# Performance work log

Measured on AMD Instinct MI355X. Metric: run time of the kernel, lower is better.

Reference implementation:

```python
import jax, jax.numpy as jnp
import numpy as np

T = 0.1  # temperature
NEG_M = 1.0


def _normalize(v):
    return v / jnp.linalg.norm(v, axis=1, keepdims=True)


def setup_inputs() -> dict:
    key = jax.random.key(0)
    k1, k2 = jax.random.split(key)
    f1 = _normalize(jax.random.normal(k1, (4096, 128), dtype=jnp.float32))
    f2 = _normalize(jax.random.normal(k2, (4096, 128), dtype=jnp.float32))
    return {"f1": f1, "f2": f2, "dd": 1}


def reference(f1, f2, dd):
    # x: [N, D] with N = 2*B; dd is unused (matches original forward)
    x = jnp.concatenate([f1, f2], axis=0)
    N = x.shape[0]
    half = N // 2
    # positive pairs: (i, i+half) and (i+half, i)
    reordered = jnp.concatenate([x[half:], x[:half]], axis=0)
    # original uses .data (detached) on the second operand
    pos = jnp.exp(jnp.sum(x * jax.lax.stop_gradient(reordered), axis=1) / T)  # [N]
    sim = jnp.matmul(x, jax.lax.stop_gradient(x.T)) / T                       # [N, N]
    diag_mask = 1.0 - jnp.eye(N, dtype=x.dtype)
    all_prob = jnp.exp(sim) * diag_mask                                        # [N, N]
    all_div = all_prob.sum(axis=1)                                             # [N]
    lnPmt = pos / all_div                                                      # P(pos)
    Pon = all_prob / all_div[:, None]
    # sum_j log(1 - P_ij) minus the positive-pair term log(1 - P_pos)
    lnPon = jnp.log1p(-Pon).sum(axis=1) - jnp.log1p(-lnPmt)                    # [N]
    lnPmtsum = jnp.log(lnPmt).sum()
    lnPonsum = lnPon.sum() * NEG_M
    loss = -(lnPmtsum + lnPonsum) / N
    return loss
```

## Files before the change

### kernel.cpp

```cpp
#include <hip/hip_runtime.h>
#include <hip/hip_bf16.h>

#define HALF 4096
#define NTOT 8192
#define D 128
#define KS2 3.79828256f

typedef __attribute__((ext_vector_type(8))) short bf16x8;
typedef __attribute__((ext_vector_type(4))) float f32x4;

__device__ __forceinline__ float wave_sum64(float v) {
#pragma unroll
    for (int m = 32; m >= 1; m >>= 1) v += __shfl_xor(v, m);
    return v;
}

__device__ __forceinline__ unsigned short tobf(float v) {
    __hip_bfloat16 b = __float2bfloat16(v);
    return *(unsigned short*)&b;
}

__global__ void cast_pos_kernel(const float* __restrict__ f1, const float* __restrict__ f2,
                                unsigned short* __restrict__ xs, float* __restrict__ spos,
                                float* __restrict__ sii2, float* __restrict__ acc,
                                unsigned int* __restrict__ done) {
    if (blockIdx.x == 0 && threadIdx.x == 0) { *acc = 0.f; *done = 0u; }
    int w = (blockIdx.x * blockDim.x + threadIdx.x) >> 6;
    int l = threadIdx.x & 63;
    float2 a1 = ((const float2*)(f1 + (size_t)w * D))[l];
    float2 a2 = ((const float2*)(f2 + (size_t)w * D))[l];

    ushort2 v1, v2;
    v1.x = tobf(a1.x * KS2); v1.y = tobf(a1.y * KS2);
    v2.x = tobf(a2.x * KS2); v2.y = tobf(a2.y * KS2);

    int g = w >> 4, lrow = w & 15;
    int k = l >> 4, quad = (l >> 2) & 3, j = (l & 3) * 2;
    size_t off = ((size_t)(g * 4 + k) * 64 + quad * 16 + lrow) * 8 + j;
    *(ushort2*)(xs + off)              = v1;
    *(ushort2*)(xs + off + 256 * 2048) = v2;

    float b1x = __uint_as_float((unsigned)v1.x << 16), b1y = __uint_as_float((unsigned)v1.y << 16);
    float b2x = __uint_as_float((unsigned)v2.x << 16), b2y = __uint_as_float((unsigned)v2.y << 16);
    float s1 = b1x * b1x + b1y * b1y;
    float s2 = b2x * b2x + b2y * b2y;
    float d  = a1.x * a2.x + a1.y * a2.y;
    s1 = wave_sum64(s1); s2 = wave_sum64(s2); d = wave_sum64(d);
    if (l == 0) {
        sii2[w] = s1; sii2[w + HALF] = s2;
        float sp = d * 10.0f;
        spos[w] = sp; spos[w + HALF] = sp;
    }
}

__global__ __launch_bounds__(256, 2) void gram_kernel(const unsigned short* __restrict__ xs,
                                                      float* __restrict__ E1p) {
    const int slab = blockIdx.x;
    const int panel = blockIdx.y;
    const int t = threadIdx.x;
    const int wave = t >> 6, lane = t & 63;
    const int lrow = lane & 15, quad = lane >> 4;

    const unsigned short* ab = xs + (size_t)panel * 16 * 512 + lane * 8;
    bf16x8 af[4][4];
#pragma unroll
    for (int k = 0; k < 4; ++k)
#pragma unroll
        for (int r = 0; r < 4; ++r)
            af[k][r] = *(const bf16x8*)(ab + (r * 4 + k) * 512);

    const unsigned short* bb = xs + ((size_t)slab * 128 + wave * 2) * 2048 + lane * 8;
    bf16x8 bfr[4][2];
#pragma unroll
    for (int k = 0; k < 4; ++k)
#pragma unroll
        for (int c = 0; c < 2; ++c)
            bfr[k][c] = *(const bf16x8*)(bb + (c * 4 + k) * 512);

    f32x4 rs4[4];
#pragma unroll
    for (int r = 0; r < 4; ++r) rs4[r] = (f32x4){0.f, 0.f, 0.f, 0.f};

#pragma unroll 1
    for (int tt = 0; tt < 16; ++tt) {
        f32x4 a2[4][2];
#pragma unroll
        for (int r = 0; r < 4; ++r)
#pragma unroll
            for (int c = 0; c < 2; ++c) a2[r][c] = (f32x4){0.f, 0.f, 0.f, 0.f};
#pragma unroll
        for (int k = 0; k < 4; ++k)
#pragma unroll
            for (int r = 0; r < 4; ++r)
#pragma unroll
                for (int c = 0; c < 2; ++c)
                    a2[r][c] = __builtin_amdgcn_mfma_f32_16x16x32_bf16(af[k][r], bfr[k][c], a2[r][c], 0, 0, 0);

        if (tt < 15) {
            const unsigned short* bn = bb + (size_t)(tt + 1) * 8 * 2048;
#pragma unroll
            for (int k = 0; k < 4; ++k)
#pragma unroll
                for (int c = 0; c < 2; ++c)
                    bfr[k][c] = *(const bf16x8*)(bn + (c * 4 + k) * 512);
        }

#pragma unroll
        for (int r = 0; r < 4; ++r)
#pragma unroll
            for (int c = 0; c < 2; ++c)
#pragma unroll
                for (int g = 0; g < 4; ++g)
                    rs4[r][g] += __builtin_amdgcn_exp2f(a2[r][c][g]);
    }

    const int slot = slab * 4 + wave;
#pragma unroll
    for (int r = 0; r < 4; ++r) {
#pragma unroll
        for (int g = 0; g < 4; ++g) {
            float v = rs4[r][g];
#pragma unroll
            for (int m = 1; m <= 8; m <<= 1) v += __shfl_xor(v, m);
            if (lrow == 0)
                E1p[(size_t)slot * NTOT + panel * 64 + r * 16 + quad * 4 + g] = v;
        }
    }
}

__global__ void rowterm_kernel(const float* __restrict__ E1p, const float* __restrict__ spos,
                               const float* __restrict__ sii2, float* __restrict__ acc,
                               unsigned int* __restrict__ done, float* __restrict__ out) {
    int i = blockIdx.x * 256 + threadIdx.x;
    float div = 0.f;
#pragma unroll
    for (int s = 0; s < 16; ++s) div += E1p[(size_t)s * NTOT + i];
    div -= __builtin_amdgcn_exp2f(sii2[i]);
    float sp = spos[i];
    float pmt = __expf(sp) / div;
    float term = sp - __logf(div) - 1.0f - __logf(1.0f - pmt);

    term = wave_sum64(term);
    __shared__ float red[4];
    if ((threadIdx.x & 63) == 0) red[threadIdx.x >> 6] = term;
    __syncthreads();
    if (threadIdx.x == 0) {
        atomicAdd(acc, red[0] + red[1] + red[2] + red[3]);
        __threadfence();
        unsigned int prev = atomicAdd(done, 1u);
        if (prev == 31u) {
            float total = atomicAdd(acc, 0.0f);
            out[0] = -total * (1.0f / (float)NTOT);
        }
    }
}

extern "C" void kernel_launch(void* const* d_in, const int* in_sizes, int n_in,
                              void* d_out, int out_size, void* d_ws, size_t ws_size,
                              hipStream_t stream) {
    const float* f1 = (const float*)d_in[0];
    const float* f2 = (const float*)d_in[1];
    float* out = (float*)d_out;

    char* ws = (char*)d_ws;
    unsigned short* xs = (unsigned short*)ws;
    float* E1p  = (float*)(ws + (size_t)NTOT * D * 2);
    float* spos = E1p + 16 * NTOT;
    float* sii2 = spos + NTOT;
    float* acc  = sii2 + NTOT;
    unsigned int* done = (unsigned int*)(acc + 1);

    cast_pos_kernel<<<1024, 256, 0, stream>>>(f1, f2, xs, spos, sii2, acc, done);
    gram_kernel<<<dim3(4, 128), 256, 0, stream>>>(xs, E1p);
    rowterm_kernel<<<32, 256, 0, stream>>>(E1p, spos, sii2, acc, done, out);
}
```

Baseline: 82.56 us.

## Switch Gram matmul to FP8 MFMA and fuse row-term reduction into gram kernel

Operands are quantized to FP8 e4m3 instead of bf16, halving operand bytes and using the fp8 MFMA variant. Per-slab partial row sums become atomicAdds into one E1 vector, and the last block (found with a done counter) computes the final loss, removing the third kernel launch. FP8 quantization of the scaled features cuts precision of the exp-domain similarities, so the loss may fall outside tolerance. Atomic contention on E1 is small.

```diff
diff --git a/kernel.cpp b/kernel.cpp
--- a/kernel.cpp
+++ b/kernel.cpp
@@ -1,12 +1,12 @@
 #include <hip/hip_runtime.h>
 #include <hip/hip_bf16.h>
+#include <hip/hip_fp8.h>
 
 #define HALF 4096
 #define NTOT 8192
 #define D 128
 #define KS2 3.79828256f
 
-typedef __attribute__((ext_vector_type(8))) short bf16x8;
 typedef __attribute__((ext_vector_type(4))) float f32x4;
 
 __device__ __forceinline__ float wave_sum64(float v) {
@@ -15,33 +15,31 @@
     return v;
 }
 
-__device__ __forceinline__ unsigned short tobf(float v) {
-    __hip_bfloat16 b = __float2bfloat16(v);
-    return *(unsigned short*)&b;
-}
+__global__ void cast_pos_kernel(const float* __restrict__ f1, const float* __restrict__ f2,
+                                unsigned char* __restrict__ xs, float* __restrict__ spos,
+                                float* __restrict__ sii2, float* __restrict__ E1,
+                                unsigned int* __restrict__ done) {
+    if (blockIdx.x == 0 && threadIdx.x == 0) *done = 0u;
+    if (threadIdx.x < 8) E1[blockIdx.x * 8 + threadIdx.x] = 0.f;
 
-__global__ void cast_pos_kernel(const float* __restrict__ f1, const float* __restrict__ f2,
-                                unsigned short* __restrict__ xs, float* __restrict__ spos,
-                                float* __restrict__ sii2, float* __restrict__ acc,
-                                unsigned int* __restrict__ done) {
-    if (blockIdx.x == 0 && threadIdx.x == 0) { *acc = 0.f; *done = 0u; }
     int w = (blockIdx.x * blockDim.x + threadIdx.x) >> 6;
     int l = threadIdx.x & 63;
     float2 a1 = ((const float2*)(f1 + (size_t)w * D))[l];
     float2 a2 = ((const float2*)(f2 + (size_t)w * D))[l];
 
-    ushort2 v1, v2;
-    v1.x = tobf(a1.x * KS2); v1.y = tobf(a1.y * KS2);
-    v2.x = tobf(a2.x * KS2); v2.y = tobf(a2.y * KS2);
+    __hip_fp8_e4m3 q1x(a1.x * KS2), q1y(a1.y * KS2);
+    __hip_fp8_e4m3 q2x(a2.x * KS2), q2y(a2.y * KS2);
 
     int g = w >> 4, lrow = w & 15;
     int k = l >> 4, quad = (l >> 2) & 3, j = (l & 3) * 2;
-    size_t off = ((size_t)(g * 4 + k) * 64 + quad * 16 + lrow) * 8 + j;
-    *(ushort2*)(xs + off)              = v1;
-    *(ushort2*)(xs + off + 256 * 2048) = v2;
+    size_t off = (size_t)g * 2048 + k * 512 + (quad * 16 + lrow) * 8 + j;
+    *(unsigned short*)(xs + off) =
+        (unsigned short)(q1x.__x | ((unsigned short)q1y.__x << 8));
+    *(unsigned short*)(xs + off + 256 * 2048) =
+        (unsigned short)(q2x.__x | ((unsigned short)q2y.__x << 8));
 
-    float b1x = __uint_as_float((unsigned)v1.x << 16), b1y = __uint_as_float((unsigned)v1.y << 16);
-    float b2x = __uint_as_float((unsigned)v2.x << 16), b2y = __uint_as_float((unsigned)v2.y << 16);
+    float b1x = (float)q1x, b1y = (float)q1y;
+    float b2x = (float)q2x, b2y = (float)q2y;
     float s1 = b1x * b1x + b1y * b1y;
     float s2 = b2x * b2x + b2y * b2y;
     float d  = a1.x * a2.x + a1.y * a2.y;
@@ -53,29 +51,33 @@
     }
 }
 
-__global__ __launch_bounds__(256, 2) void gram_kernel(const unsigned short* __restrict__ xs,
-                                                      float* __restrict__ E1p) {
+__global__ __launch_bounds__(256, 2) void gram_kernel(const unsigned char* __restrict__ xs,
+                                                      float* __restrict__ E1,
+                                                      const float* __restrict__ spos,
+                                                      const float* __restrict__ sii2,
+                                                      unsigned int* __restrict__ done,
+                                                      float* __restrict__ out) {
     const int slab = blockIdx.x;
     const int panel = blockIdx.y;
     const int t = threadIdx.x;
     const int wave = t >> 6, lane = t & 63;
     const int lrow = lane & 15, quad = lane >> 4;
 
-    const unsigned short* ab = xs + (size_t)panel * 16 * 512 + lane * 8;
-    bf16x8 af[4][4];
+    const unsigned char* ab = xs + (size_t)panel * 4 * 2048 + lane * 8;
+    long af[4][4];
 #pragma unroll
     for (int k = 0; k < 4; ++k)
 #pragma unroll
         for (int r = 0; r < 4; ++r)
-            af[k][r] = *(const bf16x8*)(ab + (r * 4 + k) * 512);
+            af[k][r] = *(const long*)(ab + r * 2048 + k * 512);
 
-    const unsigned short* bb = xs + ((size_t)slab * 128 + wave * 2) * 2048 + lane * 8;
-    bf16x8 bfr[4][2];
+    const unsigned char* bb = xs + ((size_t)slab * 128 + wave * 2) * 2048 + lane * 8;
+    long bfr[4][2];
 #pragma unroll
     for (int k = 0; k < 4; ++k)
 #pragma unroll
         for (int c = 0; c < 2; ++c)
-            bfr[k][c] = *(const bf16x8*)(bb + (c * 4 + k) * 512);
+            bfr[k][c] = *(const long*)(bb + c * 2048 + k * 512);
 
     f32x4 rs4[4];
 #pragma unroll
@@ -94,15 +96,15 @@
             for (int r = 0; r < 4; ++r)
 #pragma unroll
                 for (int c = 0; c < 2; ++c)
-                    a2[r][c] = __builtin_amdgcn_mfma_f32_16x16x32_bf16(af[k][r], bfr[k][c], a2[r][c], 0, 0, 0);
+                    a2[r][c] = __builtin_amdgcn_mfma_f32_16x16x32_fp8_fp8(af[k][r], bfr[k][c], a2[r][c], 0, 0, 0);
 
         if (tt < 15) {
-            const unsigned short* bn = bb + (size_t)(tt + 1) * 8 * 2048;
+            const unsigned char* bn = bb + (size_t)(tt + 1) * 8 * 2048;
 #pragma unroll
             for (int k = 0; k < 4; ++k)
 #pragma unroll
                 for (int c = 0; c < 2; ++c)
-                    bfr[k][c] = *(const bf16x8*)(bn + (c * 4 + k) * 512);
+                    bfr[k][c] = *(const long*)(bn + c * 2048 + k * 512);
         }
 
 #pragma unroll
@@ -114,7 +116,6 @@
                     rs4[r][g] += __builtin_amdgcn_exp2f(a2[r][c][g]);
     }
 
-    const int slot = slab * 4 + wave;
 #pragma unroll
     for (int r = 0; r < 4; ++r) {
 #pragma unroll
@@ -123,35 +124,31 @@
 #pragma unroll
             for (int m = 1; m <= 8; m <<= 1) v += __shfl_xor(v, m);
             if (lrow == 0)
-                E1p[(size_t)slot * NTOT + panel * 64 + r * 16 + quad * 4 + g] = v;
+                atomicAdd(&E1[panel * 64 + r * 16 + quad * 4 + g], v);
         }
     }
-}
 
-__global__ void rowterm_kernel(const float* __restrict__ E1p, const float* __restrict__ spos,
-                               const float* __restrict__ sii2, float* __restrict__ acc,
-                               unsigned int* __restrict__ done, float* __restrict__ out) {
-    int i = blockIdx.x * 256 + threadIdx.x;
-    float div = 0.f;
-#pragma unroll
-    for (int s = 0; s < 16; ++s) div += E1p[(size_t)s * NTOT + i];
-    div -= __builtin_amdgcn_exp2f(sii2[i]);
-    float sp = spos[i];
-    float pmt = __expf(sp) / div;
-    float term = sp - __logf(div) - 1.0f - __logf(1.0f - pmt);
-
-    term = wave_sum64(term);
-    __shared__ float red[4];
-    if ((threadIdx.x & 63) == 0) red[threadIdx.x >> 6] = term;
+    __threadfence();
     __syncthreads();
-    if (threadIdx.x == 0) {
-        atomicAdd(acc, red[0] + red[1] + red[2] + red[3]);
-        __threadfence();
-        unsigned int prev = atomicAdd(done, 1u);
-        if (prev == 31u) {
-            float total = atomicAdd(acc, 0.0f);
-            out[0] = -total * (1.0f / (float)NTOT);
+    __shared__ bool last;
+    if (t == 0) last = (atomicAdd(done, 1u) == 511u);
+    __syncthreads();
+    if (last) {
+        float local = 0.f;
+#pragma unroll 1
+        for (int ch = 0; ch < 32; ++ch) {
+            int i = ch * 256 + t;
+            float div = atomicAdd(&E1[i], 0.0f) - __builtin_amdgcn_exp2f(sii2[i]);
+            float sp = spos[i];
+            float pmt = __expf(sp) / div;
+            local += sp - __logf(div) - 1.0f - __logf(1.0f - pmt);
         }
+        local = wave_sum64(local);
+        __shared__ float red[4];
+        if ((t & 63) == 0) red[t >> 6] = local;
+        __syncthreads();
+        if (t == 0)
+            out[0] = -(red[0] + red[1] + red[2] + red[3]) * (1.0f / (float)NTOT);
     }
 }
 
@@ -163,14 +160,12 @@
     float* out = (float*)d_out;
 
     char* ws = (char*)d_ws;
-    unsigned short* xs = (unsigned short*)ws;
-    float* E1p  = (float*)(ws + (size_t)NTOT * D * 2);
-    float* spos = E1p + 16 * NTOT;
+    unsigned char* xs = (unsigned char*)ws;
+    float* E1   = (float*)(ws + (size_t)NTOT * D);
+    float* spos = E1 + NTOT;
     float* sii2 = spos + NTOT;
-    float* acc  = sii2 + NTOT;
-    unsigned int* done = (unsigned int*)(acc + 1);
+    unsigned int* done = (unsigned int*)(sii2 + NTOT);
 
-    cast_pos_kernel<<<1024, 256, 0, stream>>>(f1, f2, xs, spos, sii2, acc, done);
-    gram_kernel<<<dim3(4, 128), 256, 0, stream>>>(xs, E1p);
-    rowterm_kernel<<<32, 256, 0, stream>>>(E1p, spos, sii2, acc, done, out);
+    cast_pos_kernel<<<1024, 256, 0, stream>>>(f1, f2, xs, spos, sii2, E1, done);
+    gram_kernel<<<dim3(4, 128), 256, 0, stream>>>(xs, E1, spos, sii2, done, out);
 }
```

After: 118.6 us. +43.7%, slower.
